# Kernel optimization log

Hardware: AMD Instinct MI355X
Metric: run time of the kernel (lower is better)

Reference implementation:

```python
import jax, jax.numpy as jnp
import numpy as np

N = 100000   # nodes
E = 1600000  # edges
IN = 128
HID = 128
OUT = 64
H = 4
DH = HID // H  # 32
EPS = 1e-5


def gatconv(x, W, al, ar, b, src, dst, heads, dh, act):
    """DGL GATConv: fc -> edge attn (leaky_relu 0.2) -> segment softmax over dst -> scatter sum -> bias -> act."""
    feat = (x @ W).reshape(-1, heads, dh)            # [N,H,dh]
    el = (feat * al).sum(-1)                          # [N,H]
    er = (feat * ar).sum(-1)                          # [N,H]
    e = jax.nn.leaky_relu(el[src] + er[dst], 0.2)     # [E,H]
    m = jax.ops.segment_max(e, dst, num_segments=N)   # [N,H]
    ex = jnp.exp(e - m[dst])                          # [E,H]
    s = jax.ops.segment_sum(ex, dst, num_segments=N)  # [N,H]
    alpha = ex / s[dst]                               # [E,H]
    msg = alpha[:, :, None] * feat[src]               # [E,H,dh]
    out = jax.ops.segment_sum(msg, dst, num_segments=N)  # [N,H,dh]
    out = out + b.reshape(1, heads, dh)
    return act(out) if act is not None else out


def layernorm(x, g, beta):
    mu = x.mean(-1, keepdims=True)
    var = ((x - mu) ** 2).mean(-1, keepdims=True)
    return (x - mu) * jax.lax.rsqrt(var + EPS) * g + beta


def setup_inputs():
    key = jax.random.key(0)
    ks = jax.random.split(key, 24)
    rn = lambda k, shape, s=0.05: jax.random.normal(k, shape, dtype=jnp.float32) * s
    return {
        "x": jax.random.normal(ks[0], (N, IN), dtype=jnp.float32),
        "src": jax.random.randint(ks[1], (E,), 0, N, dtype=jnp.int32),
        "dst": jax.random.randint(ks[2], (E,), 0, N, dtype=jnp.int32),
        "W0": rn(ks[3], (IN, H * DH)), "al0": rn(ks[4], (H, DH)), "ar0": rn(ks[5], (H, DH)), "b0": jnp.zeros((H * DH,), jnp.float32),
        "W1": rn(ks[6], (HID, H * DH)), "al1": rn(ks[7], (H, DH)), "ar1": rn(ks[8], (H, DH)), "b1": jnp.zeros((H * DH,), jnp.float32),
        "W2": rn(ks[9], (HID, HID)), "al2": rn(ks[10], (1, HID)), "ar2": rn(ks[11], (1, HID)), "b2": jnp.zeros((HID,), jnp.float32),
        "g0": jnp.ones((HID,), jnp.float32), "be0": jnp.zeros((HID,), jnp.float32),
        "g1": jnp.ones((HID,), jnp.float32), "be1": jnp.zeros((HID,), jnp.float32),
        "Wc": rn(ks[12], (HID, OUT)), "bc": jnp.zeros((OUT,), jnp.float32),
    }


def reference(x, src, dst, W0, al0, ar0, b0, W1, al1, ar1, b1, W2, al2, ar2, b2,
              g0, be0, g1, be1, Wc, bc):
    # layer 0 (heads=4, elu) -> flatten -> residual -> LN (dropout in eval = identity)
    h_res = x
    h = gatconv(x, W0, al0, ar0, b0, src, dst, H, DH, jax.nn.elu).reshape(N, HID)
    h = layernorm(h + h_res, g0, be0)
    # layer 1 (heads=4, elu)
    h_res = h
    h = gatconv(h, W1, al1, ar1, b1, src, dst, H, DH, jax.nn.elu).reshape(N, HID)
    h = layernorm(h + h_res, g1, be1)
    # layer 2 (heads=1, no activation) -> squeeze -> residual, no norm
    h_res = h
    h = gatconv(h, W2, al2, ar2, b2, src, dst, 1, HID, None).reshape(N, HID)
    h = h + h_res
    embedding = h
    logits = embedding @ Wc + bc
    return (logits, embedding)
```

## Files before the change

### kernel.cpp

```cpp
#include <hip/hip_runtime.h>

#define NN 100000
#define EE 1600000
#define BSHIFT 9
#define NBKT ((NN + 511) / 512)
#define CAP 10240
#define CHUNK 2048
#define NBLKA ((EE + CHUNK - 1) / CHUNK)

typedef float f32x4 __attribute__((ext_vector_type(4)));
typedef float f32x2 __attribute__((ext_vector_type(2)));
typedef short s16x8 __attribute__((ext_vector_type(8)));

__device__ __forceinline__ ushort f2bf(float x) {
  uint u = __float_as_uint(x);
  return (ushort)((u + 0x7fffu + ((u >> 16) & 1u)) >> 16);
}
__device__ __forceinline__ uint pack2bf(float x, float y) {
  return (uint)f2bf(x) | ((uint)f2bf(y) << 16);
}
__device__ __forceinline__ float bflo(uint p) { return __uint_as_float(p << 16); }
__device__ __forceinline__ float bfhi(uint p) { return __uint_as_float(p & 0xffff0000u); }

template<int M, bool ABF, int ELER>
__global__ __launch_bounds__(256) void gemm_mfma(const void* __restrict__ Av,
    const float* __restrict__ W, const float* __restrict__ bias,
    float* __restrict__ outf, ushort* __restrict__ feat8s,
    const float* __restrict__ al, const float* __restrict__ ar,
    float* __restrict__ el, float* __restrict__ er, int N) {
  __shared__ ushort Wt[M * 136];
  const int tid = threadIdx.x;
  for (int idx = tid; idx < 128 * M; idx += 256) {
    int k = idx / M, c = idx - k * M;
    Wt[c * 136 + k] = f2bf(W[idx]);
  }
  __syncthreads();
  const int wid = tid >> 6, lane = tid & 63;
  const int rl = lane & 15, grp = lane >> 4;
  const long row0 = (long)blockIdx.x * 128;

  s16x8 af[2][4];
#pragma unroll
  for (int rt = 0; rt < 2; ++rt) {
    long row = row0 + rt * 64 + wid * 16 + rl;
    if (row >= N) row = N - 1;
    if (ABF) {
      const s16x8* Ar = (const s16x8*)((const ushort*)Av + row * 128);
#pragma unroll
      for (int ks = 0; ks < 4; ++ks) af[rt][ks] = Ar[ks * 4 + grp];
    } else {
      const float4* Ar = (const float4*)((const float*)Av + row * 128);
#pragma unroll
      for (int ks = 0; ks < 4; ++ks) {
        float4 a0 = Ar[ks * 8 + grp * 2];
        float4 a1 = Ar[ks * 8 + grp * 2 + 1];
        s16x8 f;
        f[0] = (short)f2bf(a0.x); f[1] = (short)f2bf(a0.y);
        f[2] = (short)f2bf(a0.z); f[3] = (short)f2bf(a0.w);
        f[4] = (short)f2bf(a1.x); f[5] = (short)f2bf(a1.y);
        f[6] = (short)f2bf(a1.z); f[7] = (short)f2bf(a1.w);
        af[rt][ks] = f;
      }
    }
  }
  const int NT = M / 16;
  f32x4 acc[2][NT];
#pragma unroll
  for (int rt = 0; rt < 2; ++rt)
#pragma unroll
    for (int ct = 0; ct < NT; ++ct) acc[rt][ct] = (f32x4)(0.f);

#pragma unroll
  for (int ct = 0; ct < NT; ++ct) {
#pragma unroll
    for (int ks = 0; ks < 4; ++ks) {
      s16x8 bf = *(const s16x8*)&Wt[(ct * 16 + rl) * 136 + ks * 32 + grp * 8];
      acc[0][ct] = __builtin_amdgcn_mfma_f32_16x16x32_bf16(af[0][ks], bf, acc[0][ct], 0, 0, 0);
      acc[1][ct] = __builtin_amdgcn_mfma_f32_16x16x32_bf16(af[1][ks], bf, acc[1][ct], 0, 0, 0);
    }
  }

  if (ELER > 0) __syncthreads();

#pragma unroll
  for (int rt = 0; rt < 2; ++rt) {
#pragma unroll
    for (int ct = 0; ct < NT; ++ct) {
      int col = ct * 16 + rl;
      float bb = (ELER == 0) ? bias[col] : 0.f;
#pragma unroll
      for (int j = 0; j < 4; ++j) {
        int lrow = rt * 64 + wid * 16 + grp * 4 + j;
        long grow = row0 + lrow;
        if (ELER > 0) {
          Wt[lrow * 128 + col] = f2bf(acc[rt][ct][j]);
        } else if (grow < N) {
          outf[grow * M + col] = acc[rt][ct][j] + bb;
        }
      }
    }
  }

  if (ELER > 0) {
    __syncthreads();
    const uint* stage = (const uint*)Wt;
    float2 a2 = ((const float2*)al)[lane];
    float2 r2 = ((const float2*)ar)[lane];
    for (int rr = 0; rr < 32; ++rr) {
      int lrow = wid * 32 + rr;
      long grow = row0 + lrow;
      uint p = stage[lrow * 64 + lane];
      float x0 = bflo(p), x1 = bfhi(p);
      int pk8 = __builtin_amdgcn_cvt_pk_fp8_f32(x0, x1, 0, false);
      if (grow < N) feat8s[grow * 64 + lane] = (ushort)pk8;
      float pl = x0 * a2.x + x1 * a2.y;
      float pr = x0 * r2.x + x1 * r2.y;
      if (ELER == 4) {
#pragma unroll
        for (int m = 8; m; m >>= 1) {
          pl += __shfl_xor(pl, m, 16);
          pr += __shfl_xor(pr, m, 16);
        }
        if ((lane & 15) == 0 && grow < N) {
          el[grow * 4 + (lane >> 4)] = pl;
          er[grow * 4 + (lane >> 4)] = pr;
        }
      } else {
#pragma unroll
        for (int m = 32; m; m >>= 1) {
          pl += __shfl_xor(pl, m, 64);
          pr += __shfl_xor(pr, m, 64);
        }
        if (lane == 0 && grow < N) { el[grow] = pl; er[grow] = pr; }
      }
    }
  }
}

__global__ __launch_bounds__(256) void k_partA(const int* __restrict__ src,
    const int* __restrict__ dst, uint* __restrict__ bcnt, uint* __restrict__ tmp) {
  __shared__ uint hist[NBKT], excl[NBKT], gbase[NBKT], cur[NBKT];
  __shared__ uint2 recs[CHUNK];
  const int t = threadIdx.x;
  const long e0 = (long)blockIdx.x * CHUNK;
  const int cnt = (EE - e0 < CHUNK) ? (int)(EE - e0) : CHUNK;
  for (int i = t; i < NBKT; i += 256) hist[i] = 0;
  __syncthreads();
  for (int i = t; i < cnt; i += 256) {
    int d = dst[e0 + i];
    atomicAdd(&hist[d >> BSHIFT], 1u);
  }
  __syncthreads();
  if (t == 0) {
    uint run = 0;
    for (int i = 0; i < NBKT; ++i) { excl[i] = run; run += hist[i]; }
  }
  __syncthreads();
  if (t < NBKT) {
    gbase[t] = atomicAdd(&bcnt[t], hist[t]);
    cur[t] = excl[t];
  }
  __syncthreads();
  for (int i = t; i < cnt; i += 256) {
    uint s = (uint)src[e0 + i], d = (uint)dst[e0 + i];
    uint p = atomicAdd(&cur[d >> BSHIFT], 1u);
    recs[p] = make_uint2(s, d);
  }
  __syncthreads();
  for (int i = t; i < cnt; i += 256) {
    uint2 r = recs[i];
    uint b = r.y >> BSHIFT;
    uint pos = gbase[b] + ((uint)i - excl[b]);
    if (pos < CAP) tmp[(long)b * CAP + pos] = r.x | ((r.y & 511u) << 17);
  }
}

__global__ __launch_bounds__(256) void k_bscan(const uint* __restrict__ bcnt,
    uint* __restrict__ bbase, int* __restrict__ indptr) {
  __shared__ uint lds[NBKT];
  int t = threadIdx.x;
  if (t < NBKT) lds[t] = bcnt[t];
  __syncthreads();
  if (t == 0) {
    uint run = 0;
    for (int i = 0; i < NBKT; ++i) { bbase[i] = run; run += lds[i]; }
    indptr[NN] = (int)run;
  }
}

__global__ __launch_bounds__(256) void k_partB(const uint* __restrict__ bcnt,
    const uint* __restrict__ bbase, const uint* __restrict__ tmp,
    int* __restrict__ indptr, int* __restrict__ ssrc) {
  __shared__ uint hist[512], cur[512], wsum[256];
  __shared__ uint stage[CAP];
  const int b = blockIdx.x, t = threadIdx.x;
  const int dlo = b << BSHIFT;
  const int nn = (NN - dlo < 512) ? (NN - dlo) : 512;
  int nrec = (int)bcnt[b];
  if (nrec > CAP) nrec = CAP;
  const uint base = bbase[b];
  const uint* tb = tmp + (long)b * CAP;
  for (int i = t; i < 512; i += 256) hist[i] = 0;
  __syncthreads();
  for (int i = t; i < nrec; i += 256) {
    atomicAdd(&hist[tb[i] >> 17], 1u);
  }
  __syncthreads();
  uint a0 = hist[t * 2], a1 = hist[t * 2 + 1];
  uint ts = a0 + a1;
  wsum[t] = ts;
  __syncthreads();
  for (int st = 1; st < 256; st <<= 1) {
    uint v = (t >= st) ? wsum[t - st] : 0;
    __syncthreads();
    wsum[t] += v;
    __syncthreads();
  }
  uint texcl = wsum[t] - ts;
  cur[t * 2] = texcl;
  cur[t * 2 + 1] = texcl + a0;
  if (t * 2 < nn)     indptr[dlo + t * 2]     = (int)(base + texcl);
  if (t * 2 + 1 < nn) indptr[dlo + t * 2 + 1] = (int)(base + texcl + a0);
  __syncthreads();
  for (int i = t; i < nrec; i += 256) {
    uint v = tb[i];
    uint rel = atomicAdd(&cur[v >> 17], 1u);
    stage[rel] = v;
  }
  __syncthreads();
  for (int i = t; i < nrec; i += 256) {
    ssrc[base + i] = (int)(stage[i] & 0x1FFFFu);
  }
}

template<int HEADS, bool FINAL, bool PREVBF>
__global__ __launch_bounds__(256) void gat_aggregate(
    const int* __restrict__ indptr, const int* __restrict__ ssrc,
    const char* __restrict__ el8, const float* __restrict__ er,
    const char* __restrict__ feat8, const float* __restrict__ bias,
    const void* __restrict__ prevv, const float* __restrict__ g,
    const float* __restrict__ beta, void* __restrict__ outv,
    ushort* __restrict__ embb, int N) {
  int wave = threadIdx.x >> 6, lane = threadIdx.x & 63;
  long n = (long)blockIdx.x * 4 + wave;
  if (n >= N) return;
  const int b = __builtin_amdgcn_readfirstlane(indptr[n]);
  const int e = __builtin_amdgcn_readfirstlane(indptr[n + 1]);
  const int deg = e - b;
  const int l5 = lane & 31, half = lane >> 5;
  const int head = (HEADS == 4) ? (l5 >> 3) : 0;
  const float er0 = (HEADS == 4) ? er[n * 4 + head] : er[n];
  const int* sp = ssrc + b;
  const uint lpart = (uint)l5 * 4u;
  const uint hoff = (uint)head * 4u;

  float a0 = 0.f, a1 = 0.f, a2 = 0.f, a3 = 0.f, s = 0.f;
  const int npair = (deg + 1) >> 1;
  for (int p = 0; p < npair; p += 4) {
#pragma unroll
    for (int k = 0; k < 4; ++k) {
      const int pk = p + k;
      int ja = 2 * pk;     if (ja > deg - 1) ja = deg - 1;
      int jb = 2 * pk + 1; if (jb > deg - 1) jb = deg - 1;
      uint sna = (uint)sp[ja], snb = (uint)sp[jb];
      uint fo = ((half ? snb : sna) << 7) + lpart;
      uint v = *(const uint*)(feat8 + fo);
      float elv;
      if (HEADS == 4) elv = *(const float*)(el8 + (((half ? snb : sna) << 4) + hoff));
      else            elv = *(const float*)(el8 + ((half ? snb : sna) << 2));
      float ev = elv + er0;
      ev = fmaxf(ev, 0.f) + 0.2f * fminf(ev, 0.f);
      float w = __expf(ev);
      w = (2 * pk + half < deg) ? w : 0.f;
      auto f01 = __builtin_amdgcn_cvt_pk_f32_fp8((int)v, false);
      auto f23 = __builtin_amdgcn_cvt_pk_f32_fp8((int)v, true);
      s += w;
      a0 = fmaf(w, f01[0], a0);
      a1 = fmaf(w, f01[1], a1);
      a2 = fmaf(w, f23[0], a2);
      a3 = fmaf(w, f23[1], a3);
    }
  }
  a0 += __shfl_xor(a0, 32, 64);
  a1 += __shfl_xor(a1, 32, 64);
  a2 += __shfl_xor(a2, 32, 64);
  a3 += __shfl_xor(a3, 32, 64);
  s  += __shfl_xor(s, 32, 64);

  float inv = (s > 0.f) ? 1.f / s : 0.f;
  float v0 = a0 * inv, v1 = a1 * inv, v2 = a2 * inv, v3 = a3 * inv;
  float4 bb = ((const float4*)bias)[l5];
  v0 += bb.x; v1 += bb.y; v2 += bb.z; v3 += bb.w;
  if (!FINAL) {
    v0 = v0 > 0.f ? v0 : __expf(v0) - 1.f;
    v1 = v1 > 0.f ? v1 : __expf(v1) - 1.f;
    v2 = v2 > 0.f ? v2 : __expf(v2) - 1.f;
    v3 = v3 > 0.f ? v3 : __expf(v3) - 1.f;
  }
  if (PREVBF) {
    uint2 pp = ((const uint2*)prevv)[n * 32 + l5];
    v0 += bflo(pp.x); v1 += bfhi(pp.x);
    v2 += bflo(pp.y); v3 += bfhi(pp.y);
  } else {
    float4 ph = ((const float4*)prevv)[n * 32 + l5];
    v0 += ph.x; v1 += ph.y; v2 += ph.z; v3 += ph.w;
  }
  if (!FINAL) {
    float sum = v0 + v1 + v2 + v3;
#pragma unroll
    for (int m = 16; m; m >>= 1) sum += __shfl_xor(sum, m, 64);
    float mu = sum * (1.f / 128.f);
    float d0 = v0 - mu, d1 = v1 - mu, d2 = v2 - mu, d3 = v3 - mu;
    float vs = d0 * d0 + d1 * d1 + d2 * d2 + d3 * d3;
#pragma unroll
    for (int m = 16; m; m >>= 1) vs += __shfl_xor(vs, m, 64);
    float rstd = rsqrtf(vs * (1.f / 128.f) + 1e-5f);
    float4 g4 = ((const float4*)g)[l5];
    float4 be4 = ((const float4*)beta)[l5];
    float o0 = d0 * rstd * g4.x + be4.x;
    float o1 = d1 * rstd * g4.y + be4.y;
    float o2 = d2 * rstd * g4.z + be4.z;
    float o3 = d3 * rstd * g4.w + be4.w;
    if (!half) ((uint2*)outv)[n * 32 + l5] = make_uint2(pack2bf(o0, o1), pack2bf(o2, o3));
  } else {
    if (!half) {
      ((float4*)outv)[n * 32 + l5] = make_float4(v0, v1, v2, v3);
      ((uint2*)embb)[n * 32 + l5] = make_uint2(pack2bf(v0, v1), pack2bf(v2, v3));
    }
  }
}

extern "C" void kernel_launch(void* const* d_in, const int* in_sizes, int n_in,
                              void* d_out, int out_size, void* d_ws, size_t ws_size,
                              hipStream_t stream) {
  const float* x   = (const float*)d_in[0];
  const int*   src = (const int*)d_in[1];
  const int*   dst = (const int*)d_in[2];
  const float* W0  = (const float*)d_in[3];
  const float* al0 = (const float*)d_in[4];
  const float* ar0 = (const float*)d_in[5];
  const float* b0  = (const float*)d_in[6];
  const float* W1  = (const float*)d_in[7];
  const float* al1 = (const float*)d_in[8];
  const float* ar1 = (const float*)d_in[9];
  const float* b1  = (const float*)d_in[10];
  const float* W2  = (const float*)d_in[11];
  const float* al2 = (const float*)d_in[12];
  const float* ar2 = (const float*)d_in[13];
  const float* b2  = (const float*)d_in[14];
  const float* g0  = (const float*)d_in[15];
  const float* be0 = (const float*)d_in[16];
  const float* g1  = (const float*)d_in[17];
  const float* be1 = (const float*)d_in[18];
  const float* Wc  = (const float*)d_in[19];
  const float* bc  = (const float*)d_in[20];

  float* out    = (float*)d_out;
  float* logits = out;
  float* emb    = out + (long)NN * 64;

  char*   feat8 = (char*)d_ws;
  float*  el    = (float*)(feat8 + (size_t)NN * 128);
  float*  er    = el + (long)NN * 4;
  ushort* bufAb = (ushort*)(er + (long)NN * 4);
  ushort* bufBb = bufAb + (long)NN * 128;
  uint*   tmp   = (uint*)(bufBb + (long)NN * 128);
  uint*   bcnt  = tmp + (long)NBKT * CAP;
  uint*   bbase = bcnt + NBKT;
  ushort* feat8s = (ushort*)feat8;
  char*   el8   = (char*)el;

  int* indptr = (int*)d_out;
  int* ssrc   = indptr + NN + 1;

  const int gN4 = (NN + 3) / 4;
  const int gGm = (NN + 127) / 128;

  hipMemsetAsync(bcnt, 0, NBKT * sizeof(uint), stream);
  k_partA<<<NBLKA, 256, 0, stream>>>(src, dst, bcnt, tmp);
  k_bscan<<<1, 256, 0, stream>>>(bcnt, bbase, indptr);
  k_partB<<<NBKT, 256, 0, stream>>>(bcnt, bbase, tmp, indptr, ssrc);

  gemm_mfma<128, false, 4><<<gGm, 256, 0, stream>>>(x, W0, nullptr, nullptr, feat8s, al0, ar0, el, er, NN);
  gat_aggregate<4, false, false><<<gN4, 256, 0, stream>>>(indptr, ssrc, el8, er, feat8, b0, x, g0, be0, bufAb, nullptr, NN);

  gemm_mfma<128, true, 4><<<gGm, 256, 0, stream>>>(bufAb, W1, nullptr, nullptr, feat8s, al1, ar1, el, er, NN);
  gat_aggregate<4, false, true><<<gN4, 256, 0, stream>>>(indptr, ssrc, el8, er, feat8, b1, bufAb, g1, be1, bufBb, nullptr, NN);

  gemm_mfma<128, true, 1><<<gGm, 256, 0, stream>>>(bufBb, W2, nullptr, nullptr, feat8s, al2, ar2, el, er, NN);
  gat_aggregate<1, true, true><<<gN4, 256, 0, stream>>>(indptr, ssrc, el8, er, feat8, b2, bufBb, nullptr, nullptr, emb, bufAb, NN);

  gemm_mfma<64, true, 0><<<gGm, 256, 0, stream>>>(bufAb, Wc, bc, logits, nullptr, nullptr, nullptr, nullptr, nullptr, NN);
}
```

Measured before the change: 337.1 us.

## Fold attention vectors into GEMM as extra columns via precomputed W·a

Adds a prep kernel that computes W·al and W·ar per head and appends them as extra bf16 columns to the GEMM weight tile. The attention logits el/er then come straight out of the MFMA accumulators, which removes the per-row shuffle reductions from the epilogue. The fp8 pack loop now writes 4 bytes per lane over half as many iterations, and partB masks src indices before staging rather than after. The cost is extra MFMA column tiles and more LDS per block, and el/er are now computed in bf16 instead of from the rounded feature values.

New measurement: 332.1 us. No clear change (-1.5%).

```diff
diff --git a/kernel.cpp b/kernel.cpp
--- a/kernel.cpp
+++ b/kernel.cpp
@@ -22,17 +22,48 @@
 __device__ __forceinline__ float bflo(uint p) { return __uint_as_float(p << 16); }
 __device__ __forceinline__ float bfhi(uint p) { return __uint_as_float(p & 0xffff0000u); }
 
+__global__ __launch_bounds__(256) void k_prep(const float* __restrict__ W0,
+    const float* __restrict__ al0, const float* __restrict__ ar0,
+    const float* __restrict__ W1, const float* __restrict__ al1, const float* __restrict__ ar1,
+    const float* __restrict__ W2, const float* __restrict__ al2, const float* __restrict__ ar2,
+    float* __restrict__ waug) {
+  int t = threadIdx.x;
+  for (int o = t; o < 3 * 1024; o += 256) {
+    int L = o >> 10, rem = o & 1023, c = rem >> 7, k = rem & 127;
+    const float* W = (L == 0) ? W0 : (L == 1) ? W1 : W2;
+    float v = 0.f;
+    if (L < 2) {
+      int h = c & 3;
+      const float* a = (c < 4) ? ((L == 0) ? al0 : al1) : ((L == 0) ? ar0 : ar1);
+      for (int d = 0; d < 32; ++d) v += W[k * 128 + h * 32 + d] * a[h * 32 + d];
+    } else {
+      if (c == 0)      { for (int j = 0; j < 128; ++j) v += W[k * 128 + j] * al2[j]; }
+      else if (c == 1) { for (int j = 0; j < 128; ++j) v += W[k * 128 + j] * ar2[j]; }
+    }
+    waug[o] = v;
+  }
+}
+
 template<int M, bool ABF, int ELER>
 __global__ __launch_bounds__(256) void gemm_mfma(const void* __restrict__ Av,
     const float* __restrict__ W, const float* __restrict__ bias,
     float* __restrict__ outf, ushort* __restrict__ feat8s,
-    const float* __restrict__ al, const float* __restrict__ ar,
+    const float* __restrict__ waug,
     float* __restrict__ el, float* __restrict__ er, int N) {
-  __shared__ ushort Wt[M * 136];
+  constexpr int MT = (ELER > 0) ? 144 : M;
+  constexpr int NT = MT / 16;
+  __shared__ ushort Wt[MT * 136];
   const int tid = threadIdx.x;
   for (int idx = tid; idx < 128 * M; idx += 256) {
     int k = idx / M, c = idx - k * M;
     Wt[c * 136 + k] = f2bf(W[idx]);
+  }
+  if (ELER > 0) {
+    for (int idx = tid; idx < 8 * 128; idx += 256) {
+      int c = idx >> 7, k = idx & 127;
+      Wt[(128 + c) * 136 + k] = f2bf(waug[idx]);
+      Wt[(136 + c) * 136 + k] = 0;
+    }
   }
   __syncthreads();
   const int wid = tid >> 6, lane = tid & 63;
@@ -63,7 +94,6 @@
       }
     }
   }
-  const int NT = M / 16;
   f32x4 acc[2][NT];
 #pragma unroll
   for (int rt = 0; rt < 2; ++rt)
@@ -93,7 +123,18 @@
         int lrow = rt * 64 + wid * 16 + grp * 4 + j;
         long grow = row0 + lrow;
         if (ELER > 0) {
-          Wt[lrow * 128 + col] = f2bf(acc[rt][ct][j]);
+          if (ct < 8) {
+            Wt[lrow * 128 + col] = f2bf(acc[rt][ct][j]);
+          } else if (rl < 8 && grow < N) {
+            float v = acc[rt][ct][j];
+            if (ELER == 4) {
+              if (rl < 4) el[grow * 4 + rl] = v;
+              else        er[grow * 4 + (rl - 4)] = v;
+            } else {
+              if (rl == 0)      el[grow] = v;
+              else if (rl == 1) er[grow] = v;
+            }
+          }
         } else if (grow < N) {
           outf[grow * M + col] = acc[rt][ct][j] + bb;
         }
@@ -104,35 +145,16 @@
   if (ELER > 0) {
     __syncthreads();
     const uint* stage = (const uint*)Wt;
-    float2 a2 = ((const float2*)al)[lane];
-    float2 r2 = ((const float2*)ar)[lane];
-    for (int rr = 0; rr < 32; ++rr) {
-      int lrow = wid * 32 + rr;
+    const int rhalf = lane >> 5, ei = lane & 31;
+    uint* f8u = (uint*)feat8s;
+#pragma unroll 4
+    for (int rr = 0; rr < 16; ++rr) {
+      int lrow = wid * 32 + rr * 2 + rhalf;
       long grow = row0 + lrow;
-      uint p = stage[lrow * 64 + lane];
-      float x0 = bflo(p), x1 = bfhi(p);
-      int pk8 = __builtin_amdgcn_cvt_pk_fp8_f32(x0, x1, 0, false);
-      if (grow < N) feat8s[grow * 64 + lane] = (ushort)pk8;
-      float pl = x0 * a2.x + x1 * a2.y;
-      float pr = x0 * r2.x + x1 * r2.y;
-      if (ELER == 4) {
-#pragma unroll
-        for (int m = 8; m; m >>= 1) {
-          pl += __shfl_xor(pl, m, 16);
-          pr += __shfl_xor(pr, m, 16);
-        }
-        if ((lane & 15) == 0 && grow < N) {
-          el[grow * 4 + (lane >> 4)] = pl;
-          er[grow * 4 + (lane >> 4)] = pr;
-        }
-      } else {
-#pragma unroll
-        for (int m = 32; m; m >>= 1) {
-          pl += __shfl_xor(pl, m, 64);
-          pr += __shfl_xor(pr, m, 64);
-        }
-        if (lane == 0 && grow < N) { el[grow] = pl; er[grow] = pr; }
-      }
+      uint2 pq = *(const uint2*)&stage[lrow * 64 + ei * 2];
+      int u = __builtin_amdgcn_cvt_pk_fp8_f32(bflo(pq.x), bfhi(pq.x), 0, false);
+      u = __builtin_amdgcn_cvt_pk_fp8_f32(bflo(pq.y), bfhi(pq.y), u, true);
+      if (grow < N) f8u[grow * 32 + ei] = (uint)u;
     }
   }
 }
@@ -225,11 +247,11 @@
   for (int i = t; i < nrec; i += 256) {
     uint v = tb[i];
     uint rel = atomicAdd(&cur[v >> 17], 1u);
-    stage[rel] = v;
+    stage[rel] = v & 0x1FFFFu;
   }
   __syncthreads();
   for (int i = t; i < nrec; i += 256) {
-    ssrc[base + i] = (int)(stage[i] & 0x1FFFFu);
+    ssrc[base + i] = (int)stage[i];
   }
 }
 
@@ -367,6 +389,7 @@
   uint*   tmp   = (uint*)(bufBb + (long)NN * 128);
   uint*   bcnt  = tmp + (long)NBKT * CAP;
   uint*   bbase = bcnt + NBKT;
+  float*  waug  = (float*)(bbase + NBKT);
   ushort* feat8s = (ushort*)feat8;
   char*   el8   = (char*)el;
 
@@ -376,19 +399,20 @@
   const int gN4 = (NN + 3) / 4;
   const int gGm = (NN + 127) / 128;
 
+  k_prep<<<1, 256, 0, stream>>>(W0, al0, ar0, W1, al1, ar1, W2, al2, ar2, waug);
   hipMemsetAsync(bcnt, 0, NBKT * sizeof(uint), stream);
   k_partA<<<NBLKA, 256, 0, stream>>>(src, dst, bcnt, tmp);
   k_bscan<<<1, 256, 0, stream>>>(bcnt, bbase, indptr);
   k_partB<<<NBKT, 256, 0, stream>>>(bcnt, bbase, tmp, indptr, ssrc);
 
-  gemm_mfma<128, false, 4><<<gGm, 256, 0, stream>>>(x, W0, nullptr, nullptr, feat8s, al0, ar0, el, er, NN);
+  gemm_mfma<128, false, 4><<<gGm, 256, 0, stream>>>(x, W0, nullptr, nullptr, feat8s, waug, el, er, NN);
   gat_aggregate<4, false, false><<<gN4, 256, 0, stream>>>(indptr, ssrc, el8, er, feat8, b0, x, g0, be0, bufAb, nullptr, NN);
 
-  gemm_mfma<128, true, 4><<<gGm, 256, 0, stream>>>(bufAb, W1, nullptr, nullptr, feat8s, al1, ar1, el, er, NN);
+  gemm_mfma<128, true, 4><<<gGm, 256, 0, stream>>>(bufAb, W1, nullptr, nullptr, feat8s, waug + 1024, el, er, NN);
   gat_aggregate<4, false, true><<<gN4, 256, 0, stream>>>(indptr, ssrc, el8, er, feat8, b1, bufAb, g1, be1, bufBb, nullptr, NN);
 
-  gemm_mfma<128, true, 1><<<gGm, 256, 0, stream>>>(bufBb, W2, nullptr, nullptr, feat8s, al2, ar2, el, er, NN);
+  gemm_mfma<128, true, 1><<<gGm, 256, 0, stream>>>(bufBb, W2, nullptr, nullptr, feat8s, waug + 2048, el, er, NN);
   gat_aggregate<1, true, true><<<gN4, 256, 0, stream>>>(indptr, ssrc, el8, er, feat8, b2, bufBb, nullptr, nullptr, emb, bufAb, NN);
 
-  gemm_mfma<64, true, 0><<<gGm, 256, 0, stream>>>(bufAb, Wc, bc, logits, nullptr, nullptr, nullptr, nullptr, nullptr, NN);
-}
+  gemm_mfma<64, true, 0><<<gGm, 256, 0, stream>>>(bufAb, Wc, bc, logits, nullptr, nullptr, nullptr, nullptr, NN);
+}
```
